# Performance work log

Hardware: AMD Instinct MI355X
Metric: run time of the kernel (lower is better)

The kernel has to match this reference:

```python
import jax, jax.numpy as jnp
import numpy as np
from functools import partial

N_FEATURES = 32
UNITS = [64, 32]
NUM_HEADS = 4
KEY_DIM = UNITS[-1] // NUM_HEADS  # 8
PRED_LEN = 24
B, T = 4096, 336


def _p(key, shape, scale=0.05):
    return scale * jax.random.normal(key, shape, dtype=jnp.float32)


def setup_inputs() -> dict:
    key = jax.random.key(0)
    ks = jax.random.split(key, 20)
    d = UNITS[-1]  # 32, model dim entering attention
    return {
        "x": jax.random.normal(ks[0], (B, T, N_FEATURES), dtype=jnp.float32),
        # LSTM layer 1: in=32, units=64
        "W1": _p(ks[1], (N_FEATURES, 4 * UNITS[0])),
        "U1": _p(ks[2], (UNITS[0], 4 * UNITS[0])),
        "b1": jnp.zeros((4 * UNITS[0],), jnp.float32),
        # LSTM layer 2: in=64, units=32
        "W2": _p(ks[3], (UNITS[0], 4 * UNITS[1])),
        "U2": _p(ks[4], (UNITS[1], 4 * UNITS[1])),
        "b2": jnp.zeros((4 * UNITS[1],), jnp.float32),
        # MultiHeadAttention projections (Keras layout)
        "Wq": _p(ks[5], (d, NUM_HEADS, KEY_DIM)),
        "bq": jnp.zeros((NUM_HEADS, KEY_DIM), jnp.float32),
        "Wk": _p(ks[6], (d, NUM_HEADS, KEY_DIM)),
        "bk": jnp.zeros((NUM_HEADS, KEY_DIM), jnp.float32),
        "Wv": _p(ks[7], (d, NUM_HEADS, KEY_DIM)),
        "bv": jnp.zeros((NUM_HEADS, KEY_DIM), jnp.float32),
        "Wo": _p(ks[8], (NUM_HEADS, KEY_DIM, d)),
        "bo": jnp.zeros((d,), jnp.float32),
        # Dense head
        "Wd1": _p(ks[9], (d, 64)),
        "bd1": jnp.zeros((64,), jnp.float32),
        "Wd2": _p(ks[10], (64, PRED_LEN)),
        "bd2": jnp.zeros((PRED_LEN,), jnp.float32),
    }


def _lstm(x, W, U, b, return_sequences):
    # x: [B, T, in]; Keras gate order: i, f, c(candidate), o
    Bb = x.shape[0]
    u = U.shape[0]
    x_t = jnp.swapaxes(x, 0, 1)  # [T, B, in]
    xz = x_t @ W + b             # precompute input contribution: [T, B, 4u]

    def step(carry, zx):
        h, c = carry
        z = zx + h @ U
        i, f, g, o = jnp.split(z, 4, axis=-1)
        i = jax.nn.sigmoid(i)
        f = jax.nn.sigmoid(f)
        g = jnp.tanh(g)
        o = jax.nn.sigmoid(o)
        c = f * c + i * g
        h = o * jnp.tanh(c)
        return (h, c), h

    init = (jnp.zeros((Bb, u), x.dtype), jnp.zeros((Bb, u), x.dtype))
    (h_last, _), hs = jax.lax.scan(step, init, xz)
    return jnp.swapaxes(hs, 0, 1) if return_sequences else h_last


def _mha_seq1(x, Wq, bq, Wk, bk, Wv, bv, Wo, bo):
    # x: [B, d]; attention over a seq-len-1 axis (faithful to tf.expand_dims)
    q = jnp.einsum('bd,dhk->bhk', x, Wq) + bq
    k = jnp.einsum('bd,dhk->bhk', x, Wk) + bk
    v = jnp.einsum('bd,dhk->bhk', x, Wv) + bv
    scores = jnp.sum(q * k, axis=-1, keepdims=True) / np.sqrt(KEY_DIM).astype(np.float32)  # [B,h,1]
    attn = jax.nn.softmax(scores, axis=-1)  # seq of 1 -> all ones, kept for fidelity
    o = attn * v  # [B,h,k]
    return jnp.einsum('bhk,hkd->bd', o, Wo) + bo


def reference(x, W1, U1, b1, W2, U2, b2, Wq, bq, Wk, bk, Wv, bv, Wo, bo, Wd1, bd1, Wd2, bd2):
    h = _lstm(x, W1, U1, b1, return_sequences=True)   # [B, T, 64]
    h = _lstm(h, W2, U2, b2, return_sequences=False)  # [B, 32]
    h = _mha_seq1(h, Wq, bq, Wk, bk, Wv, bv, Wo, bo)  # [B, 32]
    h = jax.nn.relu(h @ Wd1 + bd1)                    # [B, 64]
    return h @ Wd2 + bd2                              # [B, 24]
```

## Files before the change

### kernel.cpp

```cpp
#include <hip/hip_runtime.h>


#define B_TOTAL 4096
#define T_STEPS 336
#define NF      32
#define U1N     64
#define G1      256
#define U2N     32
#define G2      128
#define RROWS   8
#define NT      512
#define KH1     12
#define KG1     8
#define KH2     6
#define KG2     16

__device__ __forceinline__ float fast_sigmoid(float x) {
    return __fdividef(1.0f, 1.0f + __expf(-x));
}

__device__ __forceinline__ float fast_tanh(float x) {
    float ax = fabsf(x);
    float e  = __expf(-2.0f * ax);
    float r  = __fdividef(1.0f - e, 1.0f + e);
    return __builtin_copysignf(r, x);
}

__global__ __launch_bounds__(NT) void lstm_fused(
    const float* __restrict__ x,
    const float* __restrict__ W1, const float* __restrict__ U1, const float* __restrict__ b1,
    const float* __restrict__ W2, const float* __restrict__ U2, const float* __restrict__ b2,
    const float* __restrict__ Wv, const float* __restrict__ bv,
    const float* __restrict__ Wo, const float* __restrict__ bo,
    const float* __restrict__ Wd1, const float* __restrict__ bd1,
    const float* __restrict__ Wd2, const float* __restrict__ bd2,
    float* __restrict__ out)
{
    __shared__ float act_sh[RROWS][128];
    __shared__ float zp[RROWS * KG1 * G1];

    const int tid = threadIdx.x;
    const int r0  = blockIdx.x * RROWS;

    const int ucol = tid & 63;
    const int kg1  = tid >> 6;
    const int u2   = tid & 31;
    const int kg2  = tid >> 5;
    const int g1r  = tid >> 6, g1u = tid & 63;
    const int g2r  = tid >> 5, g2u = tid & 31;

    float4 w1w[KH1];
    #pragma unroll
    for (int j = 0; j < KH1; ++j) {
        const int kk = KH1 * kg1 + j;
        const float* row = (kk < NF) ? (W1 + kk * G1) : (U1 + (kk - NF) * G1);
        w1w[j] = make_float4(row[ucol], row[64 + ucol], row[128 + ucol], row[192 + ucol]);
    }
    float4 b1v = make_float4(0.f, 0.f, 0.f, 0.f);
    if (kg1 == 0)
        b1v = make_float4(b1[ucol], b1[64 + ucol], b1[128 + ucol], b1[192 + ucol]);

    float4 w2w[KH2];
    #pragma unroll
    for (int j = 0; j < KH2; ++j) {
        const int kk = KH2 * kg2 + j;
        const float* row = (kk < U1N) ? (W2 + kk * G2) : (U2 + (kk - U1N) * G2);
        w2w[j] = make_float4(row[u2], row[32 + u2], row[64 + u2], row[96 + u2]);
    }
    float4 b2v = make_float4(0.f, 0.f, 0.f, 0.f);
    if (kg2 == 0)
        b2v = make_float4(b2[u2], b2[32 + u2], b2[64 + u2], b2[96 + u2]);

    reinterpret_cast<float2*>(&act_sh[0][0])[tid] = make_float2(0.f, 0.f);
    float c1 = 0.f, c2 = 0.f;

    const int xbase = (r0 + g2r) * (T_STEPS * NF) + g2u;
    __syncthreads();
    if (tid < 256) act_sh[g2r][g2u] = x[xbase];
    __syncthreads();

    for (int t = 0; t < T_STEPS; ++t) {
        float xnext = 0.f;
        if (tid < 256) {
            const int tn = (t + 1 < T_STEPS) ? (t + 1) : (T_STEPS - 1);
            xnext = x[xbase + tn * NF];
        }

        {
            const int ab = KH1 * kg1;
            #pragma unroll
            for (int r = 0; r < RROWS; ++r) {
                const float4* av = reinterpret_cast<const float4*>(&act_sh[r][ab]);
                const float4 a0 = av[0], a1 = av[1], a2 = av[2];
                float a[KH1];
                a[0]=a0.x; a[1]=a0.y; a[2]=a0.z;  a[3]=a0.w;
                a[4]=a1.x; a[5]=a1.y; a[6]=a1.z;  a[7]=a1.w;
                a[8]=a2.x; a[9]=a2.y; a[10]=a2.z; a[11]=a2.w;
                float4 acc = b1v;
                #pragma unroll
                for (int j = 0; j < KH1; ++j) {
                    acc.x = fmaf(a[j], w1w[j].x, acc.x);
                    acc.y = fmaf(a[j], w1w[j].y, acc.y);
                    acc.z = fmaf(a[j], w1w[j].z, acc.z);
                    acc.w = fmaf(a[j], w1w[j].w, acc.w);
                }
                *reinterpret_cast<float4*>(&zp[(r * KG1 + kg1) * G1 + 4 * ucol]) = acc;
            }
        }
        __syncthreads();

        {
            float4 z = make_float4(0.f, 0.f, 0.f, 0.f);
            #pragma unroll
            for (int k = 0; k < KG1; ++k) {
                const float4 p = *reinterpret_cast<const float4*>(&zp[(g1r * KG1 + k) * G1 + 4 * g1u]);
                z.x += p.x; z.y += p.y; z.z += p.z; z.w += p.w;
            }
            const float ig = fast_sigmoid(z.x);
            const float fg = fast_sigmoid(z.y);
            const float gg = fast_tanh(z.z);
            const float og = fast_sigmoid(z.w);
            c1 = fmaf(fg, c1, ig * gg);
            act_sh[g1r][NF + g1u] = og * fast_tanh(c1);
            if (tid < 256) act_sh[g2r][g2u] = xnext;
        }
        __syncthreads();

        {
            const int ab = NF + KH2 * kg2;
            #pragma unroll
            for (int r = 0; r < RROWS; ++r) {
                const float2* av = reinterpret_cast<const float2*>(&act_sh[r][ab]);
                const float2 a0 = av[0], a1 = av[1], a2 = av[2];
                float a[KH2];
                a[0]=a0.x; a[1]=a0.y; a[2]=a1.x; a[3]=a1.y; a[4]=a2.x; a[5]=a2.y;
                float4 acc = b2v;
                #pragma unroll
                for (int j = 0; j < KH2; ++j) {
                    acc.x = fmaf(a[j], w2w[j].x, acc.x);
                    acc.y = fmaf(a[j], w2w[j].y, acc.y);
                    acc.z = fmaf(a[j], w2w[j].z, acc.z);
                    acc.w = fmaf(a[j], w2w[j].w, acc.w);
                }
                *reinterpret_cast<float4*>(&zp[(r * KG2 + kg2) * G2 + 4 * u2]) = acc;
            }
        }
        __syncthreads();

        if (tid < 256) {
            float4 z = make_float4(0.f, 0.f, 0.f, 0.f);
            #pragma unroll
            for (int k = 0; k < KG2; ++k) {
                const float4 p = *reinterpret_cast<const float4*>(&zp[(g2r * KG2 + k) * G2 + 4 * g2u]);
                z.x += p.x; z.y += p.y; z.z += p.z; z.w += p.w;
            }
            const float ig = fast_sigmoid(z.x);
            const float fg = fast_sigmoid(z.y);
            const float gg = fast_tanh(z.z);
            const float og = fast_sigmoid(z.w);
            c2 = fmaf(fg, c2, ig * gg);
            act_sh[g2r][96 + g2u] = og * fast_tanh(c2);
        }
        __syncthreads();
    }

    {
        float* hb = &zp[0];
        if (tid < 256) {
            float acc = bv[g2u];
            #pragma unroll
            for (int j = 0; j < 32; ++j) acc = fmaf(act_sh[g2r][96 + j], Wv[j * 32 + g2u], acc);
            hb[tid] = acc;
        }
        __syncthreads();
        if (tid < 256) {
            float acc = bo[g2u];
            #pragma unroll
            for (int j = 0; j < 32; ++j) acc = fmaf(hb[g2r * 32 + j], Wo[j * 32 + g2u], acc);
            hb[256 + tid] = acc;
        }
        __syncthreads();
        {
            float acc = bd1[g1u];
            #pragma unroll
            for (int j = 0; j < 32; ++j) acc = fmaf(hb[256 + g1r * 32 + j], Wd1[j * 64 + g1u], acc);
            hb[512 + tid] = fmaxf(acc, 0.f);
        }
        __syncthreads();
        if (tid < RROWS * 24) {
            const int rr = tid / 24, cc = tid - rr * 24;
            float acc = bd2[cc];
            #pragma unroll
            for (int j = 0; j < 64; ++j) acc = fmaf(hb[512 + rr * 64 + j], Wd2[j * 24 + cc], acc);
            out[(r0 + rr) * 24 + cc] = acc;
        }
    }
}

extern "C" void kernel_launch(void* const* d_in, const int* in_sizes, int n_in,
                              void* d_out, int out_size, void* d_ws, size_t ws_size,
                              hipStream_t stream) {
    const float* x   = (const float*)d_in[0];
    const float* W1  = (const float*)d_in[1];
    const float* U1  = (const float*)d_in[2];
    const float* b1  = (const float*)d_in[3];
    const float* W2  = (const float*)d_in[4];
    const float* U2  = (const float*)d_in[5];
    const float* b2  = (const float*)d_in[6];
    const float* Wv  = (const float*)d_in[11];
    const float* bv  = (const float*)d_in[12];
    const float* Wo  = (const float*)d_in[13];
    const float* bo  = (const float*)d_in[14];
    const float* Wd1 = (const float*)d_in[15];
    const float* bd1 = (const float*)d_in[16];
    const float* Wd2 = (const float*)d_in[17];
    const float* bd2 = (const float*)d_in[18];
    float* outp = (float*)d_out;

    hipLaunchKernelGGL(lstm_fused, dim3(B_TOTAL / RROWS), dim3(NT), 0, stream,
                       x, W1, U1, b1, W2, U2, b2, Wv, bv, Wo, bo,
                       Wd1, bd1, Wd2, bd2, outp);
}
```

Before: 1.934 ms.

## Replace shared-memory partial-sum reduction with DPP cross-lane reductions in LSTM steps

Remaps threads so the K-split partial products of each gate unit sit in adjacent lanes. They are then reduced with DPP row shuffles instead of being written to a large shared scratch buffer and summed after a barrier. This cuts the per-step barriers from four to three, drops the big shared buffer, and pads the activation rows. The cost is redundant reduction work, since every lane reduces all 8 rows and keeps only one, plus extra DPP instructions on the serial critical path.

```diff
diff --git a/kernel.cpp b/kernel.cpp
--- a/kernel.cpp
+++ b/kernel.cpp
@@ -11,9 +11,8 @@
 #define RROWS   8
 #define NT      512
 #define KH1     12
-#define KG1     8
 #define KH2     6
-#define KG2     16
+#define APAD    132
 
 __device__ __forceinline__ float fast_sigmoid(float x) {
     return __fdividef(1.0f, 1.0f + __expf(-x));
@@ -24,6 +23,27 @@
     float e  = __expf(-2.0f * ax);
     float r  = __fdividef(1.0f - e, 1.0f + e);
     return __builtin_copysignf(r, x);
+}
+
+template<int CTRL>
+__device__ __forceinline__ float dpp_add_f(float v) {
+    return v + __int_as_float(
+        __builtin_amdgcn_mov_dpp(__float_as_int(v), CTRL, 0xF, 0xF, true));
+}
+
+__device__ __forceinline__ void red8(float4& z) {
+    z.x = dpp_add_f<0xB1>(z.x);  z.y = dpp_add_f<0xB1>(z.y);
+    z.z = dpp_add_f<0xB1>(z.z);  z.w = dpp_add_f<0xB1>(z.w);
+    z.x = dpp_add_f<0x4E>(z.x);  z.y = dpp_add_f<0x4E>(z.y);
+    z.z = dpp_add_f<0x4E>(z.z);  z.w = dpp_add_f<0x4E>(z.w);
+    z.x = dpp_add_f<0x141>(z.x); z.y = dpp_add_f<0x141>(z.y);
+    z.z = dpp_add_f<0x141>(z.z); z.w = dpp_add_f<0x141>(z.w);
+}
+
+__device__ __forceinline__ void red16(float4& z) {
+    red8(z);
+    z.x = dpp_add_f<0x140>(z.x); z.y = dpp_add_f<0x140>(z.y);
+    z.z = dpp_add_f<0x140>(z.z); z.w = dpp_add_f<0x140>(z.w);
 }
 
 __global__ __launch_bounds__(NT) void lstm_fused(
@@ -36,29 +56,26 @@
     const float* __restrict__ Wd2, const float* __restrict__ bd2,
     float* __restrict__ out)
 {
-    __shared__ float act_sh[RROWS][128];
-    __shared__ float zp[RROWS * KG1 * G1];
+    __shared__ float act_sh[RROWS][APAD];
+    __shared__ float hb[1024];
 
     const int tid = threadIdx.x;
     const int r0  = blockIdx.x * RROWS;
 
-    const int ucol = tid & 63;
-    const int kg1  = tid >> 6;
-    const int u2   = tid & 31;
-    const int kg2  = tid >> 5;
-    const int g1r  = tid >> 6, g1u = tid & 63;
-    const int g2r  = tid >> 5, g2u = tid & 31;
+    const int u1  = tid >> 3;
+    const int kg1 = tid & 7;
+    const int u2  = tid >> 4;
+    const int kg2 = tid & 15;
+    const int pr  = tid >> 5, pu = tid & 31;
 
     float4 w1w[KH1];
     #pragma unroll
     for (int j = 0; j < KH1; ++j) {
         const int kk = KH1 * kg1 + j;
         const float* row = (kk < NF) ? (W1 + kk * G1) : (U1 + (kk - NF) * G1);
-        w1w[j] = make_float4(row[ucol], row[64 + ucol], row[128 + ucol], row[192 + ucol]);
-    }
-    float4 b1v = make_float4(0.f, 0.f, 0.f, 0.f);
-    if (kg1 == 0)
-        b1v = make_float4(b1[ucol], b1[64 + ucol], b1[128 + ucol], b1[192 + ucol]);
+        w1w[j] = make_float4(row[u1], row[64 + u1], row[128 + u1], row[192 + u1]);
+    }
+    const float4 b1v = make_float4(b1[u1], b1[64 + u1], b1[128 + u1], b1[192 + u1]);
 
     float4 w2w[KH2];
     #pragma unroll
@@ -67,16 +84,15 @@
         const float* row = (kk < U1N) ? (W2 + kk * G2) : (U2 + (kk - U1N) * G2);
         w2w[j] = make_float4(row[u2], row[32 + u2], row[64 + u2], row[96 + u2]);
     }
-    float4 b2v = make_float4(0.f, 0.f, 0.f, 0.f);
-    if (kg2 == 0)
-        b2v = make_float4(b2[u2], b2[32 + u2], b2[64 + u2], b2[96 + u2]);
-
-    reinterpret_cast<float2*>(&act_sh[0][0])[tid] = make_float2(0.f, 0.f);
+    const float4 b2v = make_float4(b2[u2], b2[32 + u2], b2[64 + u2], b2[96 + u2]);
+
+    for (int i = tid; i < RROWS * APAD; i += NT) (&act_sh[0][0])[i] = 0.0f;
     float c1 = 0.f, c2 = 0.f;
-
-    const int xbase = (r0 + g2r) * (T_STEPS * NF) + g2u;
+    float4 zr1 = make_float4(0.f, 0.f, 0.f, 0.f);
+    float4 zr2 = make_float4(0.f, 0.f, 0.f, 0.f);
+    const int xbase = (r0 + pr) * (T_STEPS * NF) + pu;
     __syncthreads();
-    if (tid < 256) act_sh[g2r][g2u] = x[xbase];
+    if (tid < 256) act_sh[pr][pu] = x[xbase];
     __syncthreads();
 
     for (int t = 0; t < T_STEPS; ++t) {
@@ -96,7 +112,7 @@
                 a[0]=a0.x; a[1]=a0.y; a[2]=a0.z;  a[3]=a0.w;
                 a[4]=a1.x; a[5]=a1.y; a[6]=a1.z;  a[7]=a1.w;
                 a[8]=a2.x; a[9]=a2.y; a[10]=a2.z; a[11]=a2.w;
-                float4 acc = b1v;
+                float4 acc = make_float4(0.f, 0.f, 0.f, 0.f);
                 #pragma unroll
                 for (int j = 0; j < KH1; ++j) {
                     acc.x = fmaf(a[j], w1w[j].x, acc.x);
@@ -104,26 +120,26 @@
                     acc.z = fmaf(a[j], w1w[j].z, acc.z);
                     acc.w = fmaf(a[j], w1w[j].w, acc.w);
                 }
-                *reinterpret_cast<float4*>(&zp[(r * KG1 + kg1) * G1 + 4 * ucol]) = acc;
+                red8(acc);
+                const bool keep = (kg1 == r);
+                zr1.x = keep ? acc.x : zr1.x;
+                zr1.y = keep ? acc.y : zr1.y;
+                zr1.z = keep ? acc.z : zr1.z;
+                zr1.w = keep ? acc.w : zr1.w;
             }
         }
-        __syncthreads();
-
-        {
-            float4 z = make_float4(0.f, 0.f, 0.f, 0.f);
-            #pragma unroll
-            for (int k = 0; k < KG1; ++k) {
-                const float4 p = *reinterpret_cast<const float4*>(&zp[(g1r * KG1 + k) * G1 + 4 * g1u]);
-                z.x += p.x; z.y += p.y; z.z += p.z; z.w += p.w;
-            }
-            const float ig = fast_sigmoid(z.x);
-            const float fg = fast_sigmoid(z.y);
-            const float gg = fast_tanh(z.z);
-            const float og = fast_sigmoid(z.w);
-            c1 = fmaf(fg, c1, ig * gg);
-            act_sh[g1r][NF + g1u] = og * fast_tanh(c1);
-            if (tid < 256) act_sh[g2r][g2u] = xnext;
-        }
+        float h1v;
+        {
+            const float ig = fast_sigmoid(zr1.x + b1v.x);
+            const float fg = fast_sigmoid(zr1.y + b1v.y);
+            const float gg = fast_tanh   (zr1.z + b1v.z);
+            const float og = fast_sigmoid(zr1.w + b1v.w);
+            c1  = fmaf(fg, c1, ig * gg);
+            h1v = og * fast_tanh(c1);
+        }
+        __syncthreads();
+        act_sh[kg1][NF + u1] = h1v;
+        if (tid < 256) act_sh[pr][pu] = xnext;
         __syncthreads();
 
         {
@@ -134,7 +150,7 @@
                 const float2 a0 = av[0], a1 = av[1], a2 = av[2];
                 float a[KH2];
                 a[0]=a0.x; a[1]=a0.y; a[2]=a1.x; a[3]=a1.y; a[4]=a2.x; a[5]=a2.y;
-                float4 acc = b2v;
+                float4 acc = make_float4(0.f, 0.f, 0.f, 0.f);
                 #pragma unroll
                 for (int j = 0; j < KH2; ++j) {
                     acc.x = fmaf(a[j], w2w[j].x, acc.x);
@@ -142,48 +158,48 @@
                     acc.z = fmaf(a[j], w2w[j].z, acc.z);
                     acc.w = fmaf(a[j], w2w[j].w, acc.w);
                 }
-                *reinterpret_cast<float4*>(&zp[(r * KG2 + kg2) * G2 + 4 * u2]) = acc;
+                red16(acc);
+                const bool keep = ((kg2 & 7) == r);
+                zr2.x = keep ? acc.x : zr2.x;
+                zr2.y = keep ? acc.y : zr2.y;
+                zr2.z = keep ? acc.z : zr2.z;
+                zr2.w = keep ? acc.w : zr2.w;
             }
         }
-        __syncthreads();
-
+        float h2v;
+        {
+            const float ig = fast_sigmoid(zr2.x + b2v.x);
+            const float fg = fast_sigmoid(zr2.y + b2v.y);
+            const float gg = fast_tanh   (zr2.z + b2v.z);
+            const float og = fast_sigmoid(zr2.w + b2v.w);
+            c2  = fmaf(fg, c2, ig * gg);
+            h2v = og * fast_tanh(c2);
+        }
+        __syncthreads();
+        if (kg2 < 8) act_sh[kg2][96 + u2] = h2v;
+    }
+    __syncthreads();
+
+    {
         if (tid < 256) {
-            float4 z = make_float4(0.f, 0.f, 0.f, 0.f);
-            #pragma unroll
-            for (int k = 0; k < KG2; ++k) {
-                const float4 p = *reinterpret_cast<const float4*>(&zp[(g2r * KG2 + k) * G2 + 4 * g2u]);
-                z.x += p.x; z.y += p.y; z.z += p.z; z.w += p.w;
-            }
-            const float ig = fast_sigmoid(z.x);
-            const float fg = fast_sigmoid(z.y);
-            const float gg = fast_tanh(z.z);
-            const float og = fast_sigmoid(z.w);
-            c2 = fmaf(fg, c2, ig * gg);
-            act_sh[g2r][96 + g2u] = og * fast_tanh(c2);
-        }
-        __syncthreads();
-    }
-
-    {
-        float* hb = &zp[0];
+            float acc = bv[pu];
+            #pragma unroll
+            for (int j = 0; j < 32; ++j) acc = fmaf(act_sh[pr][96 + j], Wv[j * 32 + pu], acc);
+            hb[tid] = acc;
+        }
+        __syncthreads();
         if (tid < 256) {
-            float acc = bv[g2u];
-            #pragma unroll
-            for (int j = 0; j < 32; ++j) acc = fmaf(act_sh[g2r][96 + j], Wv[j * 32 + g2u], acc);
-            hb[tid] = acc;
-        }
-        __syncthreads();
-        if (tid < 256) {
-            float acc = bo[g2u];
-            #pragma unroll
-            for (int j = 0; j < 32; ++j) acc = fmaf(hb[g2r * 32 + j], Wo[j * 32 + g2u], acc);
+            float acc = bo[pu];
+            #pragma unroll
+            for (int j = 0; j < 32; ++j) acc = fmaf(hb[pr * 32 + j], Wo[j * 32 + pu], acc);
             hb[256 + tid] = acc;
         }
         __syncthreads();
         {
-            float acc = bd1[g1u];
-            #pragma unroll
-            for (int j = 0; j < 32; ++j) acc = fmaf(hb[256 + g1r * 32 + j], Wd1[j * 64 + g1u], acc);
+            const int dr = tid >> 6, dc = tid & 63;
+            float acc = bd1[dc];
+            #pragma unroll
+            for (int j = 0; j < 32; ++j) acc = fmaf(hb[256 + dr * 32 + j], Wd1[j * 64 + dc], acc);
             hb[512 + tid] = fmaxf(acc, 0.f);
         }
         __syncthreads();
```

Measured after the change: 2.786 ms. 44.1% more time.
